# Kernel optimization log

Measured on AMD Instinct MI355X. Metric: run time of the kernel, lower is better.

Reference implementation:

```python
import jax, jax.numpy as jnp
import numpy as np
from jax import lax

EPS = 1e-5
NEG_SLOPE = 0.1
RES_SCALE = float(np.sqrt(0.5))


def upsample2x(x):
    # bilinear, align_corners=False (half-pixel), matches torch nn.Upsample(mode='bilinear')
    B, C, H, W = x.shape
    return jax.image.resize(x, (B, C, 2 * H, 2 * W), method='bilinear')


def modulated_conv2d(x, weight, styles, eps=EPS):
    # x: [B, I, H, W]; weight: [O, I, kh, kw]; styles: [B, I]
    B, I, H, W = x.shape
    O, _, kh, kw = weight.shape
    wmod = weight[None] * styles[:, None, :, None, None]            # [B,O,I,kh,kw]
    demod = lax.rsqrt(jnp.sum(wmod * wmod, axis=(2, 3, 4)) + eps)   # [B,O]
    wmod = wmod * demod[:, :, None, None, None]
    x_g = x.reshape(1, B * I, H, W)
    w_g = wmod.reshape(B * O, I, kh, kw)
    out = lax.conv_general_dilated(
        x_g, w_g, window_strides=(1, 1), padding=[(1, 1), (1, 1)],
        feature_group_count=B,
        dimension_numbers=('NCHW', 'OIHW', 'NCHW'))
    return out.reshape(B, O, H, W)


def style_block(x, w, n, conv_w, A_w, A_b, B_w, B_b, upsample):
    if upsample:
        x = upsample2x(x)
    scores = w @ A_w.T + A_b                      # [B, in_ch]
    x = modulated_conv2d(x, conv_w, scores)
    noise = n @ B_w.T + B_b                        # [B, out_ch]
    x = x + noise[:, :, None, None]
    return jnp.where(x >= 0, x, NEG_SLOPE * x)     # LeakyReLU(0.1)


def setup_inputs() -> dict:
    key = jax.random.key(0)
    ks = jax.random.split(key, 16)
    Bn, Ci, Co, Wd, Nd, H = 8, 256, 128, 512, 512, 64
    s = lambda k, shape, scale=0.05: jax.random.normal(k, shape, jnp.float32) * scale
    return {
        'x': jax.random.normal(ks[0], (Bn, Ci, H, H), jnp.float32),
        'w': jax.random.normal(ks[1], (Bn, Wd), jnp.float32),
        'n': jax.random.normal(ks[2], (Bn, Nd), jnp.float32),
        'rgb': jax.random.normal(ks[3], (Bn, 3, H, H), jnp.float32),
        'conv1_w': s(ks[4], (Ci, Ci, 3, 3)),
        'A1_w': s(ks[5], (Ci, Wd)), 'A1_b': jnp.ones((Ci,), jnp.float32),
        'B1_w': s(ks[6], (Ci, Nd)), 'B1_b': jnp.zeros((Ci,), jnp.float32),
        'conv2_w': s(ks[7], (Co, Ci, 3, 3)),
        'A2_w': s(ks[8], (Ci, Wd)), 'A2_b': jnp.ones((Ci,), jnp.float32),
        'B2_w': s(ks[9], (Co, Nd)), 'B2_b': jnp.zeros((Co,), jnp.float32),
        'rgb_w': s(ks[10], (3, Co, 1, 1)),
        'rgb_b': jnp.zeros((3,), jnp.float32),
    }


def reference(x, w, n, rgb, conv1_w, A1_w, A1_b, B1_w, B1_b,
              conv2_w, A2_w, A2_b, B2_w, B2_b, rgb_w, rgb_b):
    x = style_block(x, w, n, conv1_w, A1_w, A1_b, B1_w, B1_b, upsample=False)
    x = style_block(x, w, n, conv2_w, A2_w, A2_b, B2_w, B2_b, upsample=True)
    to_rgb = lax.conv_general_dilated(
        x, rgb_w, (1, 1), padding=[(0, 0), (0, 0)],
        dimension_numbers=('NCHW', 'OIHW', 'NCHW')) + rgb_b[None, :, None, None]
    rgb_out = (to_rgb + upsample2x(rgb)) * RES_SCALE
    return x, rgb_out
```

## Files before the change

### kernel.cpp

```cpp
#include <hip/hip_runtime.h>
#include <math.h>

#define BN 8
#define C1 256
#define C2 128
#define WD 512

typedef float  f32x4  __attribute__((ext_vector_type(4)));
typedef short  bf16x8 __attribute__((ext_vector_type(8)));
typedef unsigned short ushort_t;
typedef ushort_t us8 __attribute__((ext_vector_type(8)));
typedef ushort_t us4 __attribute__((ext_vector_type(4)));

__device__ __forceinline__ int clampi(int v, int lo, int hi) {
    return v < lo ? lo : (v > hi ? hi : v);
}
__device__ __forceinline__ float bf2f(ushort_t u) {
    return __uint_as_float(((unsigned int)u) << 16);
}
__device__ __forceinline__ ushort_t f2bf(float f) {
    unsigned int u = __float_as_uint(f);
    u = (u + 0x7fff + ((u >> 16) & 1)) >> 16;
    return (ushort_t)u;
}

__global__ __launch_bounds__(256)
void affine_kernel(const float* __restrict__ w, const float* __restrict__ n,
                   const float* __restrict__ A1w, const float* __restrict__ A1b,
                   const float* __restrict__ B1w, const float* __restrict__ B1b,
                   const float* __restrict__ A2w, const float* __restrict__ A2b,
                   const float* __restrict__ B2w, const float* __restrict__ B2b,
                   float* __restrict__ s1, float* __restrict__ s2,
                   float* __restrict__ n1, float* __restrict__ n2) {
    int tid = threadIdx.x;
    int gw = blockIdx.x * 4 + (tid >> 6);
    int lane = tid & 63;
    if (gw >= BN * 896) return;
    int b = gw / 896;
    int j = gw % 896;
    const float* vec; const float* M; const float* bias; float* out; int o;
    if (j < 256)      { o = j;       vec = w + b * WD; M = A1w; bias = A1b; out = s1 + b * 256; }
    else if (j < 512) { o = j - 256; vec = w + b * WD; M = A2w; bias = A2b; out = s2 + b * 256; }
    else if (j < 768) { o = j - 512; vec = n + b * WD; M = B1w; bias = B1b; out = n1 + b * 256; }
    else              { o = j - 768; vec = n + b * WD; M = B2w; bias = B2b; out = n2 + b * 128; }
    const float* row = M + (size_t)o * WD;
    int k0 = lane * 8;
    float4 v0 = *(const float4*)(vec + k0), v1 = *(const float4*)(vec + k0 + 4);
    float4 r0 = *(const float4*)(row + k0), r1 = *(const float4*)(row + k0 + 4);
    float acc = v0.x*r0.x + v0.y*r0.y + v0.z*r0.z + v0.w*r0.w
              + v1.x*r1.x + v1.y*r1.y + v1.z*r1.z + v1.w*r1.w;
    #pragma unroll
    for (int m = 1; m < 64; m <<= 1) acc += __shfl_xor(acc, m, 64);
    if (lane == 0) out[o] = acc + bias[o];
}

__global__ __launch_bounds__(256)
void demod_kernel(const float* __restrict__ cw1, const float* __restrict__ cw2,
                  const float* __restrict__ s1, const float* __restrict__ s2,
                  float* __restrict__ d1, float* __restrict__ d2) {
    int tid = threadIdx.x;
    int gw = blockIdx.x * 4 + (tid >> 6);
    int lane = tid & 63;
    if (gw >= BN * 384) return;
    int b = gw / 384;
    int j = gw % 384;
    const float* wbase; const float* s; float* dout; int o;
    if (j < 256) { o = j;       wbase = cw1; s = s1 + b * 256; dout = d1 + b * 256; }
    else         { o = j - 256; wbase = cw2; s = s2 + b * 256; dout = d2 + b * 128; }
    float acc = 0.f;
    #pragma unroll
    for (int i = 0; i < 4; i++) {
        int ic = lane * 4 + i;
        float sv = s[ic]; sv *= sv;
        const float* wk = wbase + ((size_t)o * 256 + ic) * 9;
        float t = 0.f;
        #pragma unroll
        for (int k = 0; k < 9; k++) t += wk[k] * wk[k];
        acc += t * sv;
    }
    #pragma unroll
    for (int m = 1; m < 64; m <<= 1) acc += __shfl_xor(acc, m, 64);
    if (lane == 0) dout[o] = rsqrtf(acc + 1e-5f);
}

__global__ __launch_bounds__(256)
void wprep_kernel(const float* __restrict__ cw1, const float* __restrict__ cw2,
                  ushort_t* __restrict__ wT1, ushort_t* __restrict__ wT2) {
    int idx = blockIdx.x * 256 + threadIdx.x;
    if (idx < 8 * 9 * 256 * 32) {
        int icw = idx & 31;
        int r = idx >> 5;
        int oc = r & 255; r >>= 8;
        int tap = r % 9, kc = r / 9;
        int ic = kc * 32 + icw;
        wT1[idx] = f2bf(cw1[((size_t)(oc * 256 + ic)) * 9 + tap]);
    } else if (idx < 589824 + 8 * 9 * 128 * 32) {
        int e = idx - 589824;
        int icw = e & 31;
        int r = e >> 5;
        int oc = r & 127; r >>= 7;
        int tap = r % 9, kc = r / 9;
        int ic = kc * 32 + icw;
        wT2[e] = f2bf(cw2[((size_t)(oc * 256 + ic)) * 9 + tap]);
    }
}

__global__ __launch_bounds__(512)
void xprep_kernel(const float* __restrict__ x, const float* __restrict__ s1,
                  ushort_t* __restrict__ xTp) {
    int tid = threadIdx.x;
    int b = blockIdx.y;
    int px_lin = blockIdx.x * 16 + (tid >> 5);
    int ic8 = tid & 31;
    const float* xb = x + (((size_t)b * C1) << 12) + px_lin;
    float4 slo = *(const float4*)(s1 + b * 256 + ic8 * 8);
    float4 shi = *(const float4*)(s1 + b * 256 + ic8 * 8 + 4);
    float sv[8] = {slo.x, slo.y, slo.z, slo.w, shi.x, shi.y, shi.z, shi.w};
    us8 h;
    #pragma unroll
    for (int j = 0; j < 8; j++) {
        float v = xb[((size_t)(ic8 * 8 + j)) << 12];
        h[j] = f2bf(v * sv[j]);
    }
    *(us8*)(xTp + ((size_t)b << 20) + (size_t)px_lin * 256 + ic8 * 8) = h;
}

__global__ __launch_bounds__(256)
void upsample_kernel(const ushort_t* __restrict__ y1T, const float* __restrict__ s2,
                     ushort_t* __restrict__ y1up) {
    int flat = blockIdx.x * 256 + threadIdx.x;
    int b = blockIdx.y;
    int ic8 = flat & 31;
    int pxl = flat >> 5;
    int ux = pxl & 127, uy = pxl >> 7;
    int jyA; float wyA;
    if (uy & 1) { jyA = uy >> 1;       wyA = 0.75f; }
    else        { jyA = (uy >> 1) - 1; wyA = 0.25f; }
    int jxA; float wxA;
    if (ux & 1) { jxA = ux >> 1;       wxA = 0.75f; }
    else        { jxA = (ux >> 1) - 1; wxA = 0.25f; }
    int yA = clampi(jyA, 0, 63), yB = clampi(jyA + 1, 0, 63);
    int xA = clampi(jxA, 0, 63), xB = clampi(jxA + 1, 0, 63);
    float wyB = 1.f - wyA, wxB = 1.f - wxA;
    const ushort_t* yb = y1T + (((size_t)b) << 20) + ic8 * 8;
    us8 qAA = *(const us8*)(yb + (size_t)(yA * 64 + xA) * 256);
    us8 qAB = *(const us8*)(yb + (size_t)(yA * 64 + xB) * 256);
    us8 qBA = *(const us8*)(yb + (size_t)(yB * 64 + xA) * 256);
    us8 qBB = *(const us8*)(yb + (size_t)(yB * 64 + xB) * 256);
    float4 slo = *(const float4*)(s2 + b * 256 + ic8 * 8);
    float4 shi = *(const float4*)(s2 + b * 256 + ic8 * 8 + 4);
    float sv[8] = {slo.x, slo.y, slo.z, slo.w, shi.x, shi.y, shi.z, shi.w};
    us8 h;
    #pragma unroll
    for (int j = 0; j < 8; j++) {
        float v = wyA * (wxA * bf2f(qAA[j]) + wxB * bf2f(qAB[j]))
                + wyB * (wxA * bf2f(qBA[j]) + wxB * bf2f(qBB[j]));
        h[j] = f2bf(v * sv[j]);
    }
    *(us8*)(y1up + ((size_t)b << 22) + (size_t)(uy * 128 + ux) * 256 + ic8 * 8) = h;
}

template<int IW, int OCTOT, int TPR, bool IS_CONV2>
__global__ __launch_bounds__(256, 2)
void conv_mfma(const ushort_t* __restrict__ inp, const ushort_t* __restrict__ wT,
               const float* __restrict__ dmod, const float* __restrict__ nza,
               ushort_t* __restrict__ outT,
               const float* __restrict__ rgb_in, const float* __restrict__ rw,
               const float* __restrict__ rb, float* __restrict__ xout,
               float* __restrict__ rgbo) {
    __shared__ __align__(16) ushort_t smem[28928];
    ushort_t* actS = smem;
    ushort_t* wS   = smem + 10432;

    const int b = blockIdx.z, ocg = blockIdx.y, tile = blockIdx.x;
    const int tyT = tile / TPR, txT = tile % TPR;
    const int ty0 = tyT * 16, tx0 = txT * 16;
    const int tid = threadIdx.x, lane = tid & 63, wave = tid >> 6;
    const int col = lane & 15, quad = lane >> 4;

    const ushort_t* inb = inp + (size_t)b * IW * IW * 256;

    int actOff[6]; bool actOk[6];
    #pragma unroll
    for (int i = 0; i < 6; i++) {
        int u = tid + 256 * i;
        int px_l = u >> 2, q = u & 3;
        int py = px_l / 18, pxx = px_l - py * 18;
        int gy = ty0 + py - 1, gx = tx0 + pxx - 1;
        bool ok = (u < 1296) && (gy >= 0) && (gy < IW) && (gx >= 0) && (gx < IW);
        actOk[i] = ok;
        actOff[i] = ok ? ((gy * IW + gx) * 256 + q * 8) : 0;
    }
    int wOff[9];
    #pragma unroll
    for (int i = 0; i < 9; i++) {
        int u = tid + 256 * i;
        int tap = u >> 8, oc = (u >> 2) & 63, q = u & 3;
        wOff[i] = (tap * OCTOT + ocg * 64 + oc) * 32 + q * 8;
    }
    const int KSTRIDE = 9 * OCTOT * 32;

    us8 aReg[6], wReg[9];
    const us8 zer = (us8)0;
#define LOADK(KC) { \
    _Pragma("unroll") for (int i = 0; i < 6; i++) \
        aReg[i] = actOk[i] ? *(const us8*)(inb + actOff[i] + (KC) * 32) : zer; \
    _Pragma("unroll") for (int i = 0; i < 9; i++) \
        wReg[i] = *(const us8*)(wT + wOff[i] + (KC) * KSTRIDE); }
#define STOREK() { \
    _Pragma("unroll") for (int i = 0; i < 6; i++) { \
        int u = tid + 256 * i; \
        if (u < 1296) *(us8*)(actS + (u & 3) * 2608 + (u >> 2) * 8) = aReg[i]; } \
    _Pragma("unroll") for (int i = 0; i < 9; i++) { \
        int u = tid + 256 * i; \
        *(us8*)(wS + (u & 3) * 4624 + (u >> 2) * 8) = wReg[i]; } }

    f32x4 acc[4][4];
    #pragma unroll
    for (int mt = 0; mt < 4; mt++)
        #pragma unroll
        for (int nt = 0; nt < 4; nt++) acc[mt][nt] = (f32x4)(0.f);

    LOADK(0);
    STOREK();
    __syncthreads();

    const ushort_t* bbase = actS + quad * 2608 + (72 * wave + col) * 8;
    const ushort_t* abase = wS + quad * 4624 + col * 8;

    for (int kc = 0; kc < 8; kc++) {
        if (kc < 7) LOADK(kc + 1);
        #pragma unroll
        for (int dx = 0; dx < 3; dx++) {
            bf16x8 bb[6];
            #pragma unroll
            for (int r = 0; r < 6; r++)
                bb[r] = *(const bf16x8*)(bbase + (r * 18 + dx) * 8);
            #pragma unroll
            for (int dy = 0; dy < 3; dy++) {
                const int tap = dy * 3 + dx;
                bf16x8 a[4];
                #pragma unroll
                for (int mt = 0; mt < 4; mt++)
                    a[mt] = *(const bf16x8*)(abase + (tap * 64 + mt * 16) * 8);
                #pragma unroll
                for (int mt = 0; mt < 4; mt++)
                    #pragma unroll
                    for (int nt = 0; nt < 4; nt++)
                        acc[mt][nt] = __builtin_amdgcn_mfma_f32_16x16x32_bf16(
                            a[mt], bb[nt + dy], acc[mt][nt], 0, 0, 0);
            }
        }
        __syncthreads();
        if (kc < 7) { STOREK(); }
        __syncthreads();
    }
#undef LOADK
#undef STOREK

    if constexpr (!IS_CONV2) {
        ushort_t* oS = smem;
        #pragma unroll
        for (int mt = 0; mt < 4; mt++) {
            int oc0 = ocg * 64 + mt * 16 + quad * 4;
            float4 dv = *(const float4*)(dmod + b * OCTOT + oc0);
            float4 nv = *(const float4*)(nza + b * OCTOT + oc0);
            float dva[4] = {dv.x, dv.y, dv.z, dv.w};
            float nva[4] = {nv.x, nv.y, nv.z, nv.w};
            #pragma unroll
            for (int nt = 0; nt < 4; nt++) {
                int px = (4 * wave + nt) * 16 + col;
                us4 h;
                #pragma unroll
                for (int r = 0; r < 4; r++) {
                    float t = acc[mt][nt][r] * dva[r] + nva[r];
                    t = (t >= 0.f) ? t : 0.1f * t;
                    h[r] = f2bf(t);
                }
                *(us4*)(oS + px * 80 + mt * 16 + quad * 4) = h;
            }
        }
        __syncthreads();
        #pragma unroll
        for (int p = 0; p < 8; p++) {
            int idx = tid + 256 * p;
            int px = idx >> 3, oc8 = idx & 7;
            us8 v = *(const us8*)(oS + px * 80 + oc8 * 8);
            int gy = ty0 + (px >> 4), gx = tx0 + (px & 15);
            *(us8*)(outT + ((size_t)b * IW * IW + gy * IW + gx) * 256 + ocg * 64 + oc8 * 8) = v;
        }
    } else {
        float dva[4][4], nva[4][4], rwa[3][4][4];
        #pragma unroll
        for (int mt = 0; mt < 4; mt++) {
            int oc0 = ocg * 64 + mt * 16 + quad * 4;
            float4 dv = *(const float4*)(dmod + b * 128 + oc0);
            float4 nv = *(const float4*)(nza + b * 128 + oc0);
            dva[mt][0] = dv.x; dva[mt][1] = dv.y; dva[mt][2] = dv.z; dva[mt][3] = dv.w;
            nva[mt][0] = nv.x; nva[mt][1] = nv.y; nva[mt][2] = nv.z; nva[mt][3] = nv.w;
            #pragma unroll
            for (int c = 0; c < 3; c++) {
                float4 rv = *(const float4*)(rw + c * 128 + oc0);
                rwa[c][mt][0] = rv.x; rwa[c][mt][1] = rv.y; rwa[c][mt][2] = rv.z; rwa[c][mt][3] = rv.w;
            }
        }
        #pragma unroll
        for (int nt = 0; nt < 4; nt++) {
            int uy = ty0 + 4 * wave + nt, ux = tx0 + col;
            float pc0 = 0.f, pc1 = 0.f, pc2 = 0.f;
            #pragma unroll
            for (int mt = 0; mt < 4; mt++) {
                int oc0 = ocg * 64 + mt * 16 + quad * 4;
                #pragma unroll
                for (int r = 0; r < 4; r++) {
                    float t = acc[mt][nt][r] * dva[mt][r] + nva[mt][r];
                    t = (t >= 0.f) ? t : 0.1f * t;
                    xout[(((size_t)b * 128 + oc0 + r) << 14) + (uy << 7) + ux] = t;
                    pc0 += rwa[0][mt][r] * t;
                    pc1 += rwa[1][mt][r] * t;
                    pc2 += rwa[2][mt][r] * t;
                }
            }
            pc0 += __shfl_xor(pc0, 16, 64); pc0 += __shfl_xor(pc0, 32, 64);
            pc1 += __shfl_xor(pc1, 16, 64); pc1 += __shfl_xor(pc1, 32, 64);
            pc2 += __shfl_xor(pc2, 16, 64); pc2 += __shfl_xor(pc2, 32, 64);
            if (quad == 0) {
                if (ocg == 0) {
                    int jyA; float wyA;
                    if (uy & 1) { jyA = uy >> 1;       wyA = 0.75f; }
                    else        { jyA = (uy >> 1) - 1; wyA = 0.25f; }
                    int jxA; float wxA;
                    if (ux & 1) { jxA = ux >> 1;       wxA = 0.75f; }
                    else        { jxA = (ux >> 1) - 1; wxA = 0.25f; }
                    int yA = clampi(jyA, 0, 63), yB = clampi(jyA + 1, 0, 63);
                    int xA = clampi(jxA, 0, 63), xB = clampi(jxA + 1, 0, 63);
                    float wyB = 1.f - wyA, wxB = 1.f - wxA;
                    const float* rp3 = rgb_in + (((size_t)b * 3) << 12);
                    #pragma unroll
                    for (int c = 0; c < 3; c++) {
                        const float* rc = rp3 + ((size_t)c << 12);
                        float up = wyA * (wxA * rc[(yA << 6) + xA] + wxB * rc[(yA << 6) + xB])
                                 + wyB * (wxA * rc[(yB << 6) + xA] + wxB * rc[(yB << 6) + xB]);
                        if (c == 0) pc0 += rb[0] + up;
                        else if (c == 1) pc1 += rb[1] + up;
                        else pc2 += rb[2] + up;
                    }
                }
                const float S = 0.70710678118654752f;
                atomicAdd(rgbo + (((size_t)b * 3 + 0) << 14) + (uy << 7) + ux, pc0 * S);
                atomicAdd(rgbo + (((size_t)b * 3 + 1) << 14) + (uy << 7) + ux, pc1 * S);
                atomicAdd(rgbo + (((size_t)b * 3 + 2) << 14) + (uy << 7) + ux, pc2 * S);
            }
        }
    }
}

extern "C" void kernel_launch(void* const* d_in, const int* in_sizes, int n_in,
                              void* d_out, int out_size, void* d_ws, size_t ws_size,
                              hipStream_t stream) {
    (void)in_sizes; (void)n_in; (void)out_size; (void)ws_size;
    const float* x     = (const float*)d_in[0];
    const float* w     = (const float*)d_in[1];
    const float* n     = (const float*)d_in[2];
    const float* rgb   = (const float*)d_in[3];
    const float* cw1   = (const float*)d_in[4];
    const float* A1w   = (const float*)d_in[5];
    const float* A1b   = (const float*)d_in[6];
    const float* B1w   = (const float*)d_in[7];
    const float* B1b   = (const float*)d_in[8];
    const float* cw2   = (const float*)d_in[9];
    const float* A2w   = (const float*)d_in[10];
    const float* A2b   = (const float*)d_in[11];
    const float* B2w   = (const float*)d_in[12];
    const float* B2b   = (const float*)d_in[13];
    const float* rgbw  = (const float*)d_in[14];
    const float* rgbb  = (const float*)d_in[15];

    char* ws = (char*)d_ws;
    float* s1 = (float*)(ws);
    float* s2 = (float*)(ws + 8192);
    float* d1 = (float*)(ws + 16384);
    float* d2 = (float*)(ws + 24576);
    float* n1 = (float*)(ws + 28672);
    float* n2 = (float*)(ws + 36864);
    ushort_t* wT1  = (ushort_t*)(ws + 40960);
    ushort_t* wT2  = (ushort_t*)(ws + 1220608);
    ushort_t* xTp  = (ushort_t*)(ws + 1810432);
    ushort_t* y1up = (ushort_t*)(ws + 18587648);
    ushort_t* y1T  = (ushort_t*)(ws + 85696512);

    float* xout = (float*)d_out;
    float* rgbo = xout + (size_t)BN * C2 * 128 * 128;

    hipMemsetAsync(rgbo, 0, (size_t)BN * 3 * 128 * 128 * 4, stream);

    affine_kernel<<<1792, 256, 0, stream>>>(w, n, A1w, A1b, B1w, B1b, A2w, A2b, B2w, B2b,
                                            s1, s2, n1, n2);
    demod_kernel<<<768, 256, 0, stream>>>(cw1, cw2, s1, s2, d1, d2);
    wprep_kernel<<<(589824 + 294912) / 256, 256, 0, stream>>>(cw1, cw2, wT1, wT2);
    xprep_kernel<<<dim3(256, BN), 512, 0, stream>>>(x, s1, xTp);
    conv_mfma<64, 256, 4, false><<<dim3(16, 4, BN), 256, 0, stream>>>(
        xTp, wT1, d1, n1, y1T, nullptr, nullptr, nullptr, nullptr, nullptr);
    upsample_kernel<<<dim3(2048, BN), 256, 0, stream>>>(y1T, s2, y1up);
    conv_mfma<128, 128, 8, true><<<dim3(64, 2, BN), 256, 0, stream>>>(
        y1up, wT2, d2, n2, nullptr, rgb, rgbw, rgbb, xout, rgbo);
}
```

Baseline: 274.1 us.

## Stream activations via global_load_lds double buffer and read weights directly into registers

The conv kernels now copy activation tiles into a double-buffered LDS area with direct global-to-LDS loads, using a zeroed scratch page in place of padding predicates. Weights are no longer staged in LDS: each lane loads its MFMA weight fragments from global memory in a new [tap][oc][ic] layout. Waves are remapped to a 2x2 split over output channels and pixels, with 2x8 accumulator tiles. This removes one barrier per K step and the register round-trip for staging. The cost is more global weight traffic per wave and higher register pressure.

```diff
diff --git a/kernel.cpp b/kernel.cpp
--- a/kernel.cpp
+++ b/kernel.cpp
@@ -11,6 +11,7 @@
 typedef unsigned short ushort_t;
 typedef ushort_t us8 __attribute__((ext_vector_type(8)));
 typedef ushort_t us4 __attribute__((ext_vector_type(4)));
+typedef unsigned int u32;
 
 __device__ __forceinline__ int clampi(int v, int lo, int hi) {
     return v < lo ? lo : (v > hi ? hi : v);
@@ -22,6 +23,11 @@
     unsigned int u = __float_as_uint(f);
     u = (u + 0x7fff + ((u >> 16) & 1)) >> 16;
     return (ushort_t)u;
+}
+__device__ __forceinline__ void gll16(const ushort_t* g, ushort_t* l) {
+    __builtin_amdgcn_global_load_lds(
+        (const __attribute__((address_space(1))) u32*)g,
+        (__attribute__((address_space(3))) u32*)l, 16, 0, 0);
 }
 
 __global__ __launch_bounds__(256)
@@ -87,20 +93,16 @@
 void wprep_kernel(const float* __restrict__ cw1, const float* __restrict__ cw2,
                   ushort_t* __restrict__ wT1, ushort_t* __restrict__ wT2) {
     int idx = blockIdx.x * 256 + threadIdx.x;
-    if (idx < 8 * 9 * 256 * 32) {
-        int icw = idx & 31;
-        int r = idx >> 5;
-        int oc = r & 255; r >>= 8;
-        int tap = r % 9, kc = r / 9;
-        int ic = kc * 32 + icw;
+    if (idx < 9 * 256 * 256) {
+        int tap = idx >> 16;
+        int oc = (idx >> 8) & 255;
+        int ic = idx & 255;
         wT1[idx] = f2bf(cw1[((size_t)(oc * 256 + ic)) * 9 + tap]);
-    } else if (idx < 589824 + 8 * 9 * 128 * 32) {
-        int e = idx - 589824;
-        int icw = e & 31;
-        int r = e >> 5;
-        int oc = r & 127; r >>= 7;
-        int tap = r % 9, kc = r / 9;
-        int ic = kc * 32 + icw;
+    } else if (idx < 9 * 256 * 256 + 9 * 128 * 256) {
+        int e = idx - 9 * 256 * 256;
+        int tap = e >> 15;
+        int oc = (e >> 8) & 127;
+        int ic = e & 255;
         wT2[e] = f2bf(cw2[((size_t)(oc * 256 + ic)) * 9 + tap]);
     }
 }
@@ -167,109 +169,89 @@
                ushort_t* __restrict__ outT,
                const float* __restrict__ rgb_in, const float* __restrict__ rw,
                const float* __restrict__ rb, float* __restrict__ xout,
-               float* __restrict__ rgbo) {
-    __shared__ __align__(16) ushort_t smem[28928];
-    ushort_t* actS = smem;
-    ushort_t* wS   = smem + 10432;
+               float* __restrict__ rgbo, const ushort_t* __restrict__ zpage) {
+    __shared__ __align__(16) ushort_t actS[2 * 10368];
 
     const int b = blockIdx.z, ocg = blockIdx.y, tile = blockIdx.x;
     const int tyT = tile / TPR, txT = tile % TPR;
     const int ty0 = tyT * 16, tx0 = txT * 16;
     const int tid = threadIdx.x, lane = tid & 63, wave = tid >> 6;
     const int col = lane & 15, quad = lane >> 4;
+    const int ochalf = wave >> 1, pxhalf = wave & 1;
 
     const ushort_t* inb = inp + (size_t)b * IW * IW * 256;
 
-    int actOff[6]; bool actOk[6];
-    #pragma unroll
-    for (int i = 0; i < 6; i++) {
-        int u = tid + 256 * i;
-        int px_l = u >> 2, q = u & 3;
-        int py = px_l / 18, pxx = px_l - py * 18;
+    const ushort_t* asrc[6];
+    #pragma unroll
+    for (int c = 0; c < 6; c++) {
+        int u = tid + 256 * c;
+        int q = u / 324, px = u - q * 324;
+        int py = px / 18, pxx = px - py * 18;
         int gy = ty0 + py - 1, gx = tx0 + pxx - 1;
         bool ok = (u < 1296) && (gy >= 0) && (gy < IW) && (gx >= 0) && (gx < IW);
-        actOk[i] = ok;
-        actOff[i] = ok ? ((gy * IW + gx) * 256 + q * 8) : 0;
-    }
-    int wOff[9];
-    #pragma unroll
-    for (int i = 0; i < 9; i++) {
-        int u = tid + 256 * i;
-        int tap = u >> 8, oc = (u >> 2) & 63, q = u & 3;
-        wOff[i] = (tap * OCTOT + ocg * 64 + oc) * 32 + q * 8;
-    }
-    const int KSTRIDE = 9 * OCTOT * 32;
-
-    us8 aReg[6], wReg[9];
-    const us8 zer = (us8)0;
-#define LOADK(KC) { \
-    _Pragma("unroll") for (int i = 0; i < 6; i++) \
-        aReg[i] = actOk[i] ? *(const us8*)(inb + actOff[i] + (KC) * 32) : zer; \
-    _Pragma("unroll") for (int i = 0; i < 9; i++) \
-        wReg[i] = *(const us8*)(wT + wOff[i] + (KC) * KSTRIDE); }
-#define STOREK() { \
-    _Pragma("unroll") for (int i = 0; i < 6; i++) { \
-        int u = tid + 256 * i; \
-        if (u < 1296) *(us8*)(actS + (u & 3) * 2608 + (u >> 2) * 8) = aReg[i]; } \
-    _Pragma("unroll") for (int i = 0; i < 9; i++) { \
-        int u = tid + 256 * i; \
-        *(us8*)(wS + (u & 3) * 4624 + (u >> 2) * 8) = wReg[i]; } }
-
-    f32x4 acc[4][4];
-    #pragma unroll
-    for (int mt = 0; mt < 4; mt++)
-        #pragma unroll
-        for (int nt = 0; nt < 4; nt++) acc[mt][nt] = (f32x4)(0.f);
-
-    LOADK(0);
-    STOREK();
+        asrc[c] = ok ? (inb + (size_t)(gy * IW + gx) * 256 + q * 8) : zpage;
+    }
+    const ushort_t* wlane = wT + (size_t)(ocg * 64 + ochalf * 32 + col) * 256 + quad * 8;
+    const int TAPSTR = OCTOT * 256;
+
+#define STAGE(NXT, KC) { \
+    ushort_t* dsb = actS + (NXT) * 10368 + (tid >> 6) * 512; \
+    _Pragma("unroll") for (int c = 0; c < 5; c++) \
+        gll16(asrc[c] + (KC) * 32, dsb + c * 2048); \
+    if (tid < 16) gll16(asrc[5] + (KC) * 32, actS + (NXT) * 10368 + 5 * 2048); }
+
+    f32x4 acc[2][8];
+    #pragma unroll
+    for (int mt = 0; mt < 2; mt++)
+        #pragma unroll
+        for (int nt = 0; nt < 8; nt++) acc[mt][nt] = (f32x4)(0.f);
+
+    STAGE(0, 0);
     __syncthreads();
 
-    const ushort_t* bbase = actS + quad * 2608 + (72 * wave + col) * 8;
-    const ushort_t* abase = wS + quad * 4624 + col * 8;
-
     for (int kc = 0; kc < 8; kc++) {
-        if (kc < 7) LOADK(kc + 1);
+        bf16x8 wf[9][2];
+        #pragma unroll
+        for (int tap = 0; tap < 9; tap++) {
+            wf[tap][0] = *(const bf16x8*)(wlane + tap * TAPSTR + kc * 32);
+            wf[tap][1] = *(const bf16x8*)(wlane + tap * TAPSTR + 16 * 256 + kc * 32);
+        }
+        if (kc < 7) STAGE((kc & 1) ^ 1, kc + 1);
+        const ushort_t* bbase = actS + (kc & 1) * 10368
+                              + (quad * 324 + pxhalf * 144 + col) * 8;
         #pragma unroll
         for (int dx = 0; dx < 3; dx++) {
-            bf16x8 bb[6];
-            #pragma unroll
-            for (int r = 0; r < 6; r++)
-                bb[r] = *(const bf16x8*)(bbase + (r * 18 + dx) * 8);
+            bf16x8 bb[10];
+            #pragma unroll
+            for (int j = 0; j < 10; j++)
+                bb[j] = *(const bf16x8*)(bbase + (j * 18 + dx) * 8);
             #pragma unroll
             for (int dy = 0; dy < 3; dy++) {
-                const int tap = dy * 3 + dx;
-                bf16x8 a[4];
                 #pragma unroll
-                for (int mt = 0; mt < 4; mt++)
-                    a[mt] = *(const bf16x8*)(abase + (tap * 64 + mt * 16) * 8);
-                #pragma unroll
-                for (int mt = 0; mt < 4; mt++)
+                for (int mt = 0; mt < 2; mt++)
                     #pragma unroll
-                    for (int nt = 0; nt < 4; nt++)
+                    for (int nt = 0; nt < 8; nt++)
                         acc[mt][nt] = __builtin_amdgcn_mfma_f32_16x16x32_bf16(
-                            a[mt], bb[nt + dy], acc[mt][nt], 0, 0, 0);
+                            wf[dy * 3 + dx][mt], bb[nt + dy], acc[mt][nt], 0, 0, 0);
             }
         }
         __syncthreads();
-        if (kc < 7) { STOREK(); }
-        __syncthreads();
-    }
-#undef LOADK
-#undef STOREK
+    }
+#undef STAGE
 
     if constexpr (!IS_CONV2) {
-        ushort_t* oS = smem;
-        #pragma unroll
-        for (int mt = 0; mt < 4; mt++) {
-            int oc0 = ocg * 64 + mt * 16 + quad * 4;
+        ushort_t* oS = actS;
+        #pragma unroll
+        for (int mt = 0; mt < 2; mt++) {
+            int ocl = ochalf * 32 + mt * 16 + quad * 4;
+            int oc0 = ocg * 64 + ocl;
             float4 dv = *(const float4*)(dmod + b * OCTOT + oc0);
             float4 nv = *(const float4*)(nza + b * OCTOT + oc0);
             float dva[4] = {dv.x, dv.y, dv.z, dv.w};
             float nva[4] = {nv.x, nv.y, nv.z, nv.w};
             #pragma unroll
-            for (int nt = 0; nt < 4; nt++) {
-                int px = (4 * wave + nt) * 16 + col;
+            for (int nt = 0; nt < 8; nt++) {
+                int px = (pxhalf * 8 + nt) * 16 + col;
                 us4 h;
                 #pragma unroll
                 for (int r = 0; r < 4; r++) {
@@ -277,7 +259,7 @@
                     t = (t >= 0.f) ? t : 0.1f * t;
                     h[r] = f2bf(t);
                 }
-                *(us4*)(oS + px * 80 + mt * 16 + quad * 4) = h;
+                *(us4*)(oS + px * 80 + ocl) = h;
             }
         }
         __syncthreads();
@@ -290,10 +272,10 @@
             *(us8*)(outT + ((size_t)b * IW * IW + gy * IW + gx) * 256 + ocg * 64 + oc8 * 8) = v;
         }
     } else {
-        float dva[4][4], nva[4][4], rwa[3][4][4];
-        #pragma unroll
-        for (int mt = 0; mt < 4; mt++) {
-            int oc0 = ocg * 64 + mt * 16 + quad * 4;
+        float dva[2][4], nva[2][4], rwa[3][2][4];
+        #pragma unroll
+        for (int mt = 0; mt < 2; mt++) {
+            int oc0 = ocg * 64 + ochalf * 32 + mt * 16 + quad * 4;
             float4 dv = *(const float4*)(dmod + b * 128 + oc0);
             float4 nv = *(const float4*)(nza + b * 128 + oc0);
             dva[mt][0] = dv.x; dva[mt][1] = dv.y; dva[mt][2] = dv.z; dva[mt][3] = dv.w;
@@ -305,12 +287,12 @@
             }
         }
         #pragma unroll
-        for (int nt = 0; nt < 4; nt++) {
-            int uy = ty0 + 4 * wave + nt, ux = tx0 + col;
+        for (int nt = 0; nt < 8; nt++) {
+            int uy = ty0 + pxhalf * 8 + nt, ux = tx0 + col;
             float pc0 = 0.f, pc1 = 0.f, pc2 = 0.f;
             #pragma unroll
-            for (int mt = 0; mt < 4; mt++) {
-                int oc0 = ocg * 64 + mt * 16 + quad * 4;
+            for (int mt = 0; mt < 2; mt++) {
+                int oc0 = ocg * 64 + ochalf * 32 + mt * 16 + quad * 4;
                 #pragma unroll
                 for (int r = 0; r < 4; r++) {
                     float t = acc[mt][nt][r] * dva[mt][r] + nva[mt][r];
@@ -325,7 +307,7 @@
             pc1 += __shfl_xor(pc1, 16, 64); pc1 += __shfl_xor(pc1, 32, 64);
             pc2 += __shfl_xor(pc2, 16, 64); pc2 += __shfl_xor(pc2, 32, 64);
             if (quad == 0) {
-                if (ocg == 0) {
+                if (ocg == 0 && ochalf == 0) {
                     int jyA; float wyA;
                     if (uy & 1) { jyA = uy >> 1;       wyA = 0.75f; }
                     else        { jyA = (uy >> 1) - 1; wyA = 0.25f; }
@@ -388,20 +370,22 @@
     ushort_t* xTp  = (ushort_t*)(ws + 1810432);
     ushort_t* y1up = (ushort_t*)(ws + 18587648);
     ushort_t* y1T  = (ushort_t*)(ws + 85696512);
+    ushort_t* zpage = (ushort_t*)(ws + 102473728);
 
     float* xout = (float*)d_out;
     float* rgbo = xout + (size_t)BN * C2 * 128 * 128;
 
+    hipMemsetAsync(zpage, 0, 4096, stream);
     hipMemsetAsync(rgbo, 0, (size_t)BN * 3 * 128 * 128 * 4, stream);
 
     affine_kernel<<<1792, 256, 0, stream>>>(w, n, A1w, A1b, B1w, B1b, A2w, A2b, B2w, B2b,
                                             s1, s2, n1, n2);
     demod_kernel<<<768, 256, 0, stream>>>(cw1, cw2, s1, s2, d1, d2);
-    wprep_kernel<<<(589824 + 294912) / 256, 256, 0, stream>>>(cw1, cw2, wT1, wT2);
+    wprep_kernel<<<(9 * 256 * 256 + 9 * 128 * 256 + 255) / 256, 256, 0, stream>>>(cw1, cw2, wT1, wT2);
     xprep_kernel<<<dim3(256, BN), 512, 0, stream>>>(x, s1, xTp);
     conv_mfma<64, 256, 4, false><<<dim3(16, 4, BN), 256, 0, stream>>>(
-        xTp, wT1, d1, n1, y1T, nullptr, nullptr, nullptr, nullptr, nullptr);
+        xTp, wT1, d1, n1, y1T, nullptr, nullptr, nullptr, nullptr, nullptr, zpage);
     upsample_kernel<<<dim3(2048, BN), 256, 0, stream>>>(y1T, s2, y1up);
     conv_mfma<128, 128, 8, true><<<dim3(64, 2, BN), 256, 0, stream>>>(
-        y1up, wT2, d2, n2, nullptr, rgb, rgbw, rgbb, xout, rgbo);
-}
+        y1up, wT2, d2, n2, nullptr, rgb, rgbw, rgbb, xout, rgbo, zpage);
+}
```

After: 334.4 us. 1.22x slower.

## Add register-prefetched double-buffered conv kernel for second modulated conv

Applied to the files above, without the earlier changes.

Adds a new conv_mfma_rp kernel for the second conv that keeps each wave's 3x3 weight fragments in registers, loaded straight from a new tap-major weight layout. Activations are double-buffered in LDS with a register prefetch of the next K chunk, so only one barrier is needed per chunk. Each wave owns 16 output channels across all 256 pixels and reuses LDS rows across the dy taps. The rgb bilinear residual is now added only by wave 0 of ocg 0, which fixes duplicate adds in the multi-wave case. The cost is higher register pressure (weights plus prefetch plus 16 accumulators), which may limit occupancy.

```diff
diff --git a/kernel.cpp b/kernel.cpp
--- a/kernel.cpp
+++ b/kernel.cpp
@@ -11,6 +11,7 @@
 typedef unsigned short ushort_t;
 typedef ushort_t us8 __attribute__((ext_vector_type(8)));
 typedef ushort_t us4 __attribute__((ext_vector_type(4)));
+typedef unsigned int u32;
 
 __device__ __forceinline__ int clampi(int v, int lo, int hi) {
     return v < lo ? lo : (v > hi ? hi : v);
@@ -94,13 +95,11 @@
         int tap = r % 9, kc = r / 9;
         int ic = kc * 32 + icw;
         wT1[idx] = f2bf(cw1[((size_t)(oc * 256 + ic)) * 9 + tap]);
-    } else if (idx < 589824 + 8 * 9 * 128 * 32) {
+    } else if (idx < 589824 + 9 * 128 * 256) {
         int e = idx - 589824;
-        int icw = e & 31;
-        int r = e >> 5;
-        int oc = r & 127; r >>= 7;
-        int tap = r % 9, kc = r / 9;
-        int ic = kc * 32 + icw;
+        int tap = e >> 15;
+        int oc = (e >> 8) & 127;
+        int ic = e & 255;
         wT2[e] = f2bf(cw2[((size_t)(oc * 256 + ic)) * 9 + tap]);
     }
 }
@@ -162,12 +161,12 @@
 
 template<int IW, int OCTOT, int TPR, bool IS_CONV2>
 __global__ __launch_bounds__(256, 2)
-void conv_mfma(const ushort_t* __restrict__ inp, const ushort_t* __restrict__ wT,
-               const float* __restrict__ dmod, const float* __restrict__ nza,
-               ushort_t* __restrict__ outT,
-               const float* __restrict__ rgb_in, const float* __restrict__ rw,
-               const float* __restrict__ rb, float* __restrict__ xout,
-               float* __restrict__ rgbo) {
+void conv_mfma_ls(const ushort_t* __restrict__ inp, const ushort_t* __restrict__ wT,
+                  const float* __restrict__ dmod, const float* __restrict__ nza,
+                  ushort_t* __restrict__ outT,
+                  const float* __restrict__ rgb_in, const float* __restrict__ rw,
+                  const float* __restrict__ rb, float* __restrict__ xout,
+                  float* __restrict__ rgbo) {
     __shared__ __align__(16) ushort_t smem[28928];
     ushort_t* actS = smem;
     ushort_t* wS   = smem + 10432;
@@ -325,7 +324,7 @@
             pc1 += __shfl_xor(pc1, 16, 64); pc1 += __shfl_xor(pc1, 32, 64);
             pc2 += __shfl_xor(pc2, 16, 64); pc2 += __shfl_xor(pc2, 32, 64);
             if (quad == 0) {
-                if (ocg == 0) {
+                if (ocg == 0 && wave == 0) {
                     int jyA; float wyA;
                     if (uy & 1) { jyA = uy >> 1;       wyA = 0.75f; }
                     else        { jyA = (uy >> 1) - 1; wyA = 0.25f; }
@@ -355,6 +354,182 @@
     }
 }
 
+template<int IW, int OCTOT, int TPR, bool IS_CONV2>
+__global__ __launch_bounds__(256, 2)
+void conv_mfma_rp(const ushort_t* __restrict__ inp, const ushort_t* __restrict__ wT,
+                  const float* __restrict__ dmod, const float* __restrict__ nza,
+                  ushort_t* __restrict__ outT,
+                  const float* __restrict__ rgb_in, const float* __restrict__ rw,
+                  const float* __restrict__ rb, float* __restrict__ xout,
+                  float* __restrict__ rgbo) {
+    __shared__ __align__(16) ushort_t actS[2 * 10368];
+
+    const int b = blockIdx.z, ocg = blockIdx.y, tile = blockIdx.x;
+    const int tyT = tile / TPR, txT = tile % TPR;
+    const int ty0 = tyT * 16, tx0 = txT * 16;
+    const int tid = threadIdx.x, lane = tid & 63, wave = tid >> 6;
+    const int col = lane & 15, quad = lane >> 4;
+
+    const ushort_t* inb = inp + (size_t)b * IW * IW * 256;
+
+    int actOff[6]; bool actOk[6]; int ldsOff[6];
+    #pragma unroll
+    for (int c = 0; c < 6; c++) {
+        int u = tid + 256 * c;
+        int px_l = u >> 2, q = u & 3;
+        int py = px_l / 18, pxx = px_l - py * 18;
+        int gy = ty0 + py - 1, gx = tx0 + pxx - 1;
+        bool ok = (u < 1296) && (gy >= 0) && (gy < IW) && (gx >= 0) && (gx < IW);
+        actOk[c] = ok;
+        actOff[c] = ok ? ((gy * IW + gx) * 256 + q * 8) : 0;
+        ldsOff[c] = (q * 324 + px_l) * 8;
+    }
+    const ushort_t* wlane = wT + (size_t)(ocg * 64 + wave * 16 + col) * 256 + quad * 8;
+    const int TAPSTR = OCTOT * 256;
+
+    us8 aReg[6];
+    const us8 zer = (us8)0;
+#define LOADK(KC) { \
+    _Pragma("unroll") for (int c = 0; c < 6; c++) \
+        aReg[c] = actOk[c] ? *(const us8*)(inb + actOff[c] + (KC) * 32) : zer; }
+#define STOREK(BUF) { \
+    _Pragma("unroll") for (int c = 0; c < 6; c++) { \
+        int u = tid + 256 * c; \
+        if (u < 1296) *(us8*)(actS + (BUF) * 10368 + ldsOff[c]) = aReg[c]; } }
+
+    f32x4 acc[16];
+    #pragma unroll
+    for (int nt = 0; nt < 16; nt++) acc[nt] = (f32x4)(0.f);
+
+    bf16x8 wf[9], wfN[9];
+    LOADK(0);
+    #pragma unroll
+    for (int t = 0; t < 9; t++) wf[t] = *(const bf16x8*)(wlane + t * TAPSTR);
+    STOREK(0);
+    __syncthreads();
+
+    for (int kc = 0; kc < 8; kc++) {
+        if (kc < 7) {
+            LOADK(kc + 1);
+            #pragma unroll
+            for (int t = 0; t < 9; t++)
+                wfN[t] = *(const bf16x8*)(wlane + t * TAPSTR + (kc + 1) * 32);
+        }
+        const ushort_t* bbase = actS + (kc & 1) * 10368 + (quad * 324 + col) * 8;
+        #pragma unroll
+        for (int h = 0; h < 2; h++) {
+            #pragma unroll
+            for (int dx = 0; dx < 3; dx++) {
+                bf16x8 bb[10];
+                #pragma unroll
+                for (int j = 0; j < 10; j++)
+                    bb[j] = *(const bf16x8*)(bbase + ((h * 8 + j) * 18 + dx) * 8);
+                #pragma unroll
+                for (int dy = 0; dy < 3; dy++)
+                    #pragma unroll
+                    for (int nt = 0; nt < 8; nt++)
+                        acc[h * 8 + nt] = __builtin_amdgcn_mfma_f32_16x16x32_bf16(
+                            wf[dy * 3 + dx], bb[nt + dy], acc[h * 8 + nt], 0, 0, 0);
+            }
+        }
+        if (kc < 7) STOREK((kc & 1) ^ 1);
+        __syncthreads();
+        if (kc < 7) {
+            #pragma unroll
+            for (int t = 0; t < 9; t++) wf[t] = wfN[t];
+        }
+    }
+#undef LOADK
+#undef STOREK
+
+    if constexpr (!IS_CONV2) {
+        ushort_t* oS = actS;
+        const int ocl = wave * 16 + quad * 4;
+        const int oc0 = ocg * 64 + ocl;
+        float4 dv = *(const float4*)(dmod + b * OCTOT + oc0);
+        float4 nv = *(const float4*)(nza + b * OCTOT + oc0);
+        float dva[4] = {dv.x, dv.y, dv.z, dv.w};
+        float nva[4] = {nv.x, nv.y, nv.z, nv.w};
+        #pragma unroll
+        for (int nt = 0; nt < 16; nt++) {
+            int px = nt * 16 + col;
+            us4 h;
+            #pragma unroll
+            for (int r = 0; r < 4; r++) {
+                float t = acc[nt][r] * dva[r] + nva[r];
+                t = (t >= 0.f) ? t : 0.1f * t;
+                h[r] = f2bf(t);
+            }
+            *(us4*)(oS + px * 80 + ocl) = h;
+        }
+        __syncthreads();
+        #pragma unroll
+        for (int p = 0; p < 8; p++) {
+            int idx = tid + 256 * p;
+            int px = idx >> 3, oc8 = idx & 7;
+            us8 v = *(const us8*)(oS + px * 80 + oc8 * 8);
+            int gy = ty0 + (px >> 4), gx = tx0 + (px & 15);
+            *(us8*)(outT + ((size_t)b * IW * IW + gy * IW + gx) * 256 + ocg * 64 + oc8 * 8) = v;
+        }
+    } else {
+        const int oc0 = ocg * 64 + wave * 16 + quad * 4;
+        float4 dv = *(const float4*)(dmod + b * 128 + oc0);
+        float4 nv = *(const float4*)(nza + b * 128 + oc0);
+        float dva[4] = {dv.x, dv.y, dv.z, dv.w};
+        float nva[4] = {nv.x, nv.y, nv.z, nv.w};
+        float rwa[3][4];
+        #pragma unroll
+        for (int c = 0; c < 3; c++) {
+            float4 rv = *(const float4*)(rw + c * 128 + oc0);
+            rwa[c][0] = rv.x; rwa[c][1] = rv.y; rwa[c][2] = rv.z; rwa[c][3] = rv.w;
+        }
+        #pragma unroll
+        for (int nt = 0; nt < 16; nt++) {
+            int uy = ty0 + nt, ux = tx0 + col;
+            float pc0 = 0.f, pc1 = 0.f, pc2 = 0.f;
+            #pragma unroll
+            for (int r = 0; r < 4; r++) {
+                float t = acc[nt][r] * dva[r] + nva[r];
+                t = (t >= 0.f) ? t : 0.1f * t;
+                xout[(((size_t)b * 128 + oc0 + r) << 14) + (uy << 7) + ux] = t;
+                pc0 += rwa[0][r] * t;
+                pc1 += rwa[1][r] * t;
+                pc2 += rwa[2][r] * t;
+            }
+            pc0 += __shfl_xor(pc0, 16, 64); pc0 += __shfl_xor(pc0, 32, 64);
+            pc1 += __shfl_xor(pc1, 16, 64); pc1 += __shfl_xor(pc1, 32, 64);
+            pc2 += __shfl_xor(pc2, 16, 64); pc2 += __shfl_xor(pc2, 32, 64);
+            if (quad == 0) {
+                if (ocg == 0 && wave == 0) {
+                    int jyA; float wyA;
+                    if (uy & 1) { jyA = uy >> 1;       wyA = 0.75f; }
+                    else        { jyA = (uy >> 1) - 1; wyA = 0.25f; }
+                    int jxA; float wxA;
+                    if (ux & 1) { jxA = ux >> 1;       wxA = 0.75f; }
+                    else        { jxA = (ux >> 1) - 1; wxA = 0.25f; }
+                    int yA = clampi(jyA, 0, 63), yB = clampi(jyA + 1, 0, 63);
+                    int xA = clampi(jxA, 0, 63), xB = clampi(jxA + 1, 0, 63);
+                    float wyB = 1.f - wyA, wxB = 1.f - wxA;
+                    const float* rp3 = rgb_in + (((size_t)b * 3) << 12);
+                    #pragma unroll
+                    for (int c = 0; c < 3; c++) {
+                        const float* rc = rp3 + ((size_t)c << 12);
+                        float up = wyA * (wxA * rc[(yA << 6) + xA] + wxB * rc[(yA << 6) + xB])
+                                 + wyB * (wxA * rc[(yB << 6) + xA] + wxB * rc[(yB << 6) + xB]);
+                        if (c == 0) pc0 += rb[0] + up;
+                        else if (c == 1) pc1 += rb[1] + up;
+                        else pc2 += rb[2] + up;
+                    }
+                }
+                const float S = 0.70710678118654752f;
+                atomicAdd(rgbo + (((size_t)b * 3 + 0) << 14) + (uy << 7) + ux, pc0 * S);
+                atomicAdd(rgbo + (((size_t)b * 3 + 1) << 14) + (uy << 7) + ux, pc1 * S);
+                atomicAdd(rgbo + (((size_t)b * 3 + 2) << 14) + (uy << 7) + ux, pc2 * S);
+            }
+        }
+    }
+}
+
 extern "C" void kernel_launch(void* const* d_in, const int* in_sizes, int n_in,
                               void* d_out, int out_size, void* d_ws, size_t ws_size,
                               hipStream_t stream) {
@@ -399,9 +574,9 @@
     demod_kernel<<<768, 256, 0, stream>>>(cw1, cw2, s1, s2, d1, d2);
     wprep_kernel<<<(589824 + 294912) / 256, 256, 0, stream>>>(cw1, cw2, wT1, wT2);
     xprep_kernel<<<dim3(256, BN), 512, 0, stream>>>(x, s1, xTp);
-    conv_mfma<64, 256, 4, false><<<dim3(16, 4, BN), 256, 0, stream>>>(
+    conv_mfma_ls<64, 256, 4, false><<<dim3(16, 4, BN), 256, 0, stream>>>(
         xTp, wT1, d1, n1, y1T, nullptr, nullptr, nullptr, nullptr, nullptr);
     upsample_kernel<<<dim3(2048, BN), 256, 0, stream>>>(y1T, s2, y1up);
-    conv_mfma<128, 128, 8, true><<<dim3(64, 2, BN), 256, 0, stream>>>(
+    conv_mfma_rp<128, 128, 8, true><<<dim3(64, 2, BN), 256, 0, stream>>>(
         y1up, wT2, d2, n2, nullptr, rgb, rgbw, rgbb, xout, rgbo);
 }
```

Result: slower. 283.6 us (+3.5%).
